# Kernel tuning notes

Measured on AMD Instinct MI355X. Metric: run time of the kernel, lower is better.

Reference implementation:

```python
import jax, jax.numpy as jnp
import numpy as np

VOCAB, EMB, HID, OUT = 1000, 256, 512, 1
NUM_IN, NUM_OUT = 7, 4
B, S = 64, 512
D = EMB + NUM_OUT  # conv input dim = 260


def setup_inputs() -> dict:
    key = jax.random.key(0)
    ks = jax.random.split(key, 8)
    ev = jax.random.randint(ks[0], (B, S, 1), 0, VOCAB).astype(jnp.float32)
    num = jax.random.normal(ks[1], (B, S, NUM_IN), jnp.float32)
    X = jnp.concatenate([ev, num], axis=-1)  # [B,S,8]; col 0 = event ids
    def w(k, shape, fan_in):
        return jax.random.normal(k, shape, jnp.float32) / np.sqrt(fan_in).astype(np.float32)
    return {
        "X": X,
        "emb": w(ks[2], (VOCAB, EMB), EMB),
        "Wn": w(ks[3], (NUM_IN, NUM_OUT), NUM_IN), "bn": jnp.zeros((NUM_OUT,), jnp.float32),
        "Wf": w(ks[4], (D, 3 * HID), D), "bf": jnp.zeros((3 * HID,), jnp.float32),
        "Wb": w(ks[5], (D, 3 * HID), D), "bb": jnp.zeros((3 * HID,), jnp.float32),
        "Wo": w(ks[6], (2 * HID, OUT), 2 * HID), "bo": jnp.zeros((OUT,), jnp.float32),
    }


def _fo_pool(Z, F):
    # Z, F: [S, B, H]. Linear recurrence h_t = F_t * h_{t-1} + (1 - F_t) * Z_t.
    def step(h, zf):
        z, f = zf
        h = f * h + (1.0 - f) * z
        return h, h
    h0 = jnp.zeros(Z.shape[1:], Z.dtype)
    _, hs = jax.lax.scan(step, h0, (Z, F))
    return hs  # [S, B, H]


def _forward(X, emb, Wn, bn, Wf, bf, Wb, bb, Wo, bo):
    ev = jax.lax.stop_gradient(X[:, :, 0]).astype(jnp.int32)  # event-type ids
    num = X[:, :, 1:]
    e = emb[ev]                          # [B,S,EMB]
    n = num @ Wn + bn                    # [B,S,NUM_OUT]
    c = jnp.concatenate([e, n], axis=-1)  # [B,S,D]

    def gates(W, b):
        g = jnp.einsum('bsd,dk->sbk', c, W) + b  # kernel-1 conv == GEMM; [S,B,3H]
        Z, F = g[..., :HID], g[..., HID:2 * HID]  # O gate is computed but unused upstream
        return jnp.tanh(Z), jax.nn.sigmoid(F)

    Zf, Ff = gates(Wf, bf)
    Zb, Fb = gates(Wb, bb)
    hf = _fo_pool(Zf, Ff)                       # forward direction
    hb = _fo_pool(Zb[::-1], Fb[::-1])[::-1]     # backward: scan reversed, re-reverse
    # torch takes h_combined[-1]: last forward state, first backward-scan state
    final = jnp.concatenate([hf[-1], hb[-1]], axis=-1)  # [B, 2H]
    return final @ Wo + bo  # dropout p=0 is identity


def reference(X, emb, Wn, bn, Wf, bf, Wb, bb, Wo, bo):
    return _forward(X, emb, Wn, bn, Wf, bf, Wb, bb, Wo, bo)
```

## Files before the change

### kernel.cpp

```cpp
#include <hip/hip_runtime.h>
#include <stdint.h>

#define B_ 64
#define S_ 512
#define EMB_ 256
#define NIN_ 7
#define NOUT_ 4
#define HID_ 512
#define VOCAB_ 1000
#define VP_ 1024
#define NG_ 2048

typedef __bf16 bf16x8 __attribute__((ext_vector_type(8)));
typedef float floatx4 __attribute__((ext_vector_type(4)));
typedef unsigned short u16x8 __attribute__((ext_vector_type(8)));

__device__ __forceinline__ unsigned short f2bf(float f) {
    unsigned u = __float_as_uint(f);
    u += 0x7FFFu + ((u >> 16) & 1u);
    return (unsigned short)(u >> 16);
}
__device__ __forceinline__ float bf2f(unsigned short h) {
    return __uint_as_float(((unsigned)h) << 16);
}
__device__ __forceinline__ float rcp_(float x) { return __builtin_amdgcn_rcpf(x); }
__device__ __forceinline__ float exp2_(float x) {
    float r; asm("v_exp_f32 %0, %1" : "=v"(r) : "v"(x)); return r;
}
#define L2E_ 1.4426950408889634f
__device__ __forceinline__ float sigmoidf_(float x) {
    return rcp_(1.0f + exp2_(x * (-L2E_)));
}
__device__ __forceinline__ float tanhf_(float x) {
    float ax = fabsf(x);
    float e = exp2_(ax * (-2.0f * L2E_));
    float t = (1.0f - e) * rcp_(1.0f + e);
    return copysignf(t, x);
}


__global__ __launch_bounds__(256) void prep(
    const float* __restrict__ emb, const float* __restrict__ bn,
    const float* __restrict__ Wf, const float* __restrict__ bfv,
    const float* __restrict__ Wb, const float* __restrict__ bb,
    unsigned short* __restrict__ Aemb, unsigned short* __restrict__ WT,
    float* __restrict__ W4, float* __restrict__ bvec) {
    int bid = blockIdx.x;
    int tid = threadIdx.x;

    if (bid < 64) {
        int g = bid;
#pragma unroll
        for (int half = 0; half < 2; ++half) {
            int t = tid + 256 * half;
            int r15 = t & 15;
            int kchunk = (t >> 4) & 3;
            int kt = t >> 6;
            int row = g * 16 + r15;
            int k0 = kt * 32 + kchunk * 8;
            unsigned short p[8];
            if (row < VOCAB_) {
                float4 a = *(const float4*)(emb + (size_t)row * EMB_ + k0);
                float4 b = *(const float4*)(emb + (size_t)row * EMB_ + k0 + 4);
                p[0]=f2bf(a.x); p[1]=f2bf(a.y); p[2]=f2bf(a.z); p[3]=f2bf(a.w);
                p[4]=f2bf(b.x); p[5]=f2bf(b.y); p[6]=f2bf(b.z); p[7]=f2bf(b.w);
            } else {
#pragma unroll
                for (int q = 0; q < 8; ++q) p[q] = 0;
            }
            size_t chunk = ((size_t)(g >> 3) * 8 + kt) * 8 + (g & 7);
            *(u16x8*)(Aemb + chunk * 512 + (16 * kchunk + r15) * 8) =
                *(const u16x8*)p;
        }
    } else if (bid < 192) {
        __shared__ float raw[32][132];
        int job = bid - 64;
        int idx = job >> 3;
        int kt  = job & 7;
        int p = idx >> 3;
        int gq = idx & 7;
        const float* W = p ? Wb : Wf;
        int j0 = gq * 64;
        int r = tid >> 3;
        int i = tid & 7;
        int k0 = kt * 32;

        const float* src = W + (size_t)(k0 + r) * 1536;
        float4 a0 = *(const float4*)(src + j0 + i * 8);
        float4 a1 = *(const float4*)(src + j0 + i * 8 + 4);
        float4 b0 = *(const float4*)(src + 512 + j0 + i * 8);
        float4 b1 = *(const float4*)(src + 512 + j0 + i * 8 + 4);
        *(float4*)&raw[r][i * 8]          = a0;
        *(float4*)&raw[r][i * 8 + 4]      = a1;
        *(float4*)&raw[r][64 + i * 8]     = b0;
        *(float4*)&raw[r][64 + i * 8 + 4] = b1;
        __syncthreads();
#pragma unroll
        for (int h = 0; h < 2; ++h) {
            int e = tid + 256 * h;
            int gl = e >> 6;
            int rest = e & 63;
            int kchunk = rest >> 4;
            int v15 = rest & 15;
            int joff = gl * 8 + (v15 >> 1);
            int cl = joff + 64 * (v15 & 1);
            unsigned short pk[8];
#pragma unroll
            for (int q = 0; q < 8; ++q) pk[q] = f2bf(raw[kchunk * 8 + q][cl]);
            int g = p * 64 + gq * 8 + gl;
            size_t chunk = ((size_t)(g >> 3) * 8 + kt) * 8 + (g & 7);
            *(u16x8*)(WT + chunk * 512 + (16 * kchunk + v15) * 8) =
                *(const u16x8*)pk;
        }
    } else {
        int v = (bid - 192) * 256 + tid;
        int part = v >> 10;
        int m = v & 1023;
        int j = m >> 1;
        int c = (m & 1) ? (512 + j) : j;
        const float* W = part ? Wb : Wf;
        float bv = part ? bb[c] : bfv[c];
#pragma unroll
        for (int q = 0; q < NOUT_; ++q) {
            float w = W[(size_t)(256 + q) * 1536 + c];
            W4[(size_t)q * NG_ + v] = w;
            bv = fmaf(bn[q], w, bv);
        }
        bvec[v] = bv;
    }
}

__global__ __launch_bounds__(256) void gemmG(
    const unsigned short* __restrict__ Aemb, const unsigned short* __restrict__ WT,
    const float* __restrict__ bvec, unsigned short* __restrict__ G) {
    int bid = blockIdx.x;
    int mtile = bid & 7;
    int ntile = bid >> 3;
    int r0 = mtile * 128;
    int n0 = ntile * 128;
    int tid = threadIdx.x;
    int lane = tid & 63, wave = tid >> 6;
    int wm = wave & 1, wn = wave >> 1;
    int rl = lane & 15;

    const unsigned short* pa = Aemb + ((size_t)mtile * 64 + 4 * wm) * 512 + lane * 8;
    const unsigned short* pb = WT + ((size_t)ntile * 64 + 4 * wn) * 512 + lane * 8;

    floatx4 acc[4][4];
#pragma unroll
    for (int mi = 0; mi < 4; ++mi)
#pragma unroll
        for (int ni = 0; ni < 4; ++ni) acc[mi][ni] = (floatx4){0.f, 0.f, 0.f, 0.f};

    bf16x8 afc[4], bfc[4], afn[4], bfn[4];
#pragma unroll
    for (int mi = 0; mi < 4; ++mi) afc[mi] = *(const bf16x8*)(pa + mi * 512);
#pragma unroll
    for (int ni = 0; ni < 4; ++ni) bfc[ni] = *(const bf16x8*)(pb + ni * 512);

#pragma unroll
    for (int kt = 0; kt < 8; ++kt) {
        if (kt < 7) {
#pragma unroll
            for (int mi = 0; mi < 4; ++mi)
                afn[mi] = *(const bf16x8*)(pa + (size_t)(kt + 1) * 4096 + mi * 512);
#pragma unroll
            for (int ni = 0; ni < 4; ++ni)
                bfn[ni] = *(const bf16x8*)(pb + (size_t)(kt + 1) * 4096 + ni * 512);
        }
#pragma unroll
        for (int mi = 0; mi < 4; ++mi)
#pragma unroll
            for (int ni = 0; ni < 4; ++ni)
                acc[mi][ni] = __builtin_amdgcn_mfma_f32_16x16x32_bf16(afc[mi], bfc[ni], acc[mi][ni], 0, 0, 0);
        if (kt < 7) {
#pragma unroll
            for (int mi = 0; mi < 4; ++mi) afc[mi] = afn[mi];
#pragma unroll
            for (int ni = 0; ni < 4; ++ni) bfc[ni] = bfn[ni];
        }
    }

#pragma unroll
    for (int ni = 0; ni < 4; ++ni) {
        int n = n0 + 64 * wn + 16 * ni + rl;
        float bv = bvec[n];
#pragma unroll
        for (int mi = 0; mi < 4; ++mi) {
            int rb = r0 + 64 * wm + 16 * mi + (lane >> 4) * 4;
#pragma unroll
            for (int v = 0; v < 4; ++v)
                G[(size_t)(rb + v) * NG_ + n] = f2bf(acc[mi][ni][v] + bv);
        }
    }
}

__global__ __launch_bounds__(512) void scan(
    const float* __restrict__ X, const unsigned short* __restrict__ G,
    const float* __restrict__ W4, const float* __restrict__ Wn,
    float* __restrict__ PQ) {
    __shared__ float LX[512];
    __shared__ float LN[64][4];
    __shared__ int   LO[64];
    int bid = blockIdx.x;
    int b = bid >> 3, chunk = bid & 7;
    int s0 = chunk * 64;
    int j = threadIdx.x;

    LX[j] = X[((size_t)b * S_ + s0 + (j >> 3)) * 8 + (j & 7)];
    __syncthreads();

    if (j < 64) LO[j] = (int)LX[j * 8] * (NG_ * 2);
    if (j < 256) {
        int t = j >> 2, q = j & 3;
        float s = 0.f;
#pragma unroll
        for (int i = 0; i < NIN_; ++i) s = fmaf(LX[t * 8 + 1 + i], Wn[i * NOUT_ + q], s);
        LN[t][q] = s;
    }

    float2 w4p[NOUT_];
#pragma unroll
    for (int q = 0; q < NOUT_; ++q)
        w4p[q] = *(const float2*)(W4 + (size_t)q * NG_ + 2 * j);
    __syncthreads();

    const char* Gb = (const char*)G + 4 * j;
    unsigned gp[8];
#pragma unroll
    for (int r = 0; r < 8; ++r)
        gp[r] = *(const unsigned*)(Gb + LO[r]);

    float P = 1.f, Q = 0.f;
#pragma unroll 8
    for (int s = 0; s < 64; ++s) {
        unsigned gpc = gp[s & 7];
        if (s < 56)
            gp[s & 7] = *(const unsigned*)(Gb + LO[s + 8]);
        float gz = bf2f((unsigned short)(gpc & 0xffffu));
        float gf = bf2f((unsigned short)(gpc >> 16));
        float4 n4 = *(const float4*)(&LN[s][0]);
        gz = fmaf(n4.x, w4p[0].x, gz);
        gz = fmaf(n4.y, w4p[1].x, gz);
        gz = fmaf(n4.z, w4p[2].x, gz);
        gz = fmaf(n4.w, w4p[3].x, gz);
        gf = fmaf(n4.x, w4p[0].y, gf);
        gf = fmaf(n4.y, w4p[1].y, gf);
        gf = fmaf(n4.z, w4p[2].y, gf);
        gf = fmaf(n4.w, w4p[3].y, gf);
        float z = tanhf_(gz);
        float f = sigmoidf_(gf);
        Q = fmaf(f, Q - z, z);
        P *= f;
    }
    ((float2*)PQ)[(size_t)bid * 512 + j] = make_float2(P, Q);
}

__global__ __launch_bounds__(512) void final_out(
    const float* __restrict__ X, const unsigned short* __restrict__ G,
    const float* __restrict__ W4, const float* __restrict__ Wn,
    const float* __restrict__ Wo, const float* __restrict__ bo,
    const float* __restrict__ PQ, float* __restrict__ out) {
    int b = blockIdx.x;
    int j = threadIdx.x;

    float h = 0.f;
#pragma unroll
    for (int c = 0; c < 8; ++c) {
        float2 pq = ((const float2*)PQ)[((size_t)b * 8 + c) * 512 + j];
        h = fmaf(pq.x, h, pq.y);
    }

    const float* xr = X + ((size_t)b * S_ + (S_ - 1)) * 8;
    int ev = (int)xr[0];
    float n4[NOUT_];
#pragma unroll
    for (int q = 0; q < NOUT_; ++q) {
        float s = 0.f;
#pragma unroll
        for (int i = 0; i < NIN_; ++i) s = fmaf(xr[1 + i], Wn[i * NOUT_ + q], s);
        n4[q] = s;
    }
    unsigned gpc = *(const unsigned*)(G + (size_t)ev * NG_ + 1024 + 2 * j);
    float gz = bf2f((unsigned short)(gpc & 0xffffu));
    float gf = bf2f((unsigned short)(gpc >> 16));
#pragma unroll
    for (int q = 0; q < NOUT_; ++q) {
        float2 w = *(const float2*)(W4 + (size_t)q * NG_ + 1024 + 2 * j);
        gz = fmaf(n4[q], w.x, gz);
        gf = fmaf(n4[q], w.y, gf);
    }
    float hb = (1.f - sigmoidf_(gf)) * tanhf_(gz);

    float partial = fmaf(h, Wo[j], hb * Wo[512 + j]);
#pragma unroll
    for (int off = 32; off > 0; off >>= 1)
        partial += __shfl_down(partial, off);
    __shared__ float red[8];
    if ((j & 63) == 0) red[j >> 6] = partial;
    __syncthreads();
    if (j == 0) {
        float s = bo[0];
#pragma unroll
        for (int w = 0; w < 8; ++w) s += red[w];
        out[b] = s;
    }
}

extern "C" void kernel_launch(void* const* d_in, const int* in_sizes, int n_in,
                              void* d_out, int out_size, void* d_ws, size_t ws_size,
                              hipStream_t stream) {
    const float* X   = (const float*)d_in[0];
    const float* emb = (const float*)d_in[1];
    const float* Wn  = (const float*)d_in[2];
    const float* bn  = (const float*)d_in[3];
    const float* Wf  = (const float*)d_in[4];
    const float* bfv = (const float*)d_in[5];
    const float* Wb  = (const float*)d_in[6];
    const float* bb  = (const float*)d_in[7];
    const float* Wo  = (const float*)d_in[8];
    const float* bo  = (const float*)d_in[9];
    float* out = (float*)d_out;

    size_t off_A  = 0;
    size_t off_WT = off_A  + (size_t)VP_ * EMB_ * 2;
    size_t off_G  = off_WT + (size_t)NG_ * EMB_ * 2;
    size_t off_W4 = off_G  + (size_t)VP_ * NG_ * 2;
    size_t off_bv = off_W4 + (size_t)NOUT_ * NG_ * 4;
    size_t off_PQ = off_bv + (size_t)NG_ * 4;
    size_t need   = off_PQ + (size_t)B_ * 8 * 512 * 2 * sizeof(float);
    if (ws_size < need) return;

    unsigned short* Aemb = (unsigned short*)((char*)d_ws + off_A);
    unsigned short* WT   = (unsigned short*)((char*)d_ws + off_WT);
    unsigned short* G    = (unsigned short*)((char*)d_ws + off_G);
    float*          W4   = (float*)((char*)d_ws + off_W4);
    float*          bvec = (float*)((char*)d_ws + off_bv);
    float*          PQ   = (float*)((char*)d_ws + off_PQ);

    prep<<<200, 256, 0, stream>>>(emb, bn, Wf, bfv, Wb, bb, Aemb, WT, W4, bvec);
    gemmG<<<128, 256, 0, stream>>>(Aemb, WT, bvec, G);
    scan<<<512, 512, 0, stream>>>(X, G, W4, Wn, PQ);
    final_out<<<64, 512, 0, stream>>>(X, G, W4, Wn, Wo, bo, PQ, out);
}
```

Baseline: 110.9 us.

## Compute backward gates only for final tokens and fuse final reduction into scan

```diff
diff --git a/kernel.cpp b/kernel.cpp
--- a/kernel.cpp
+++ b/kernel.cpp
@@ -14,6 +14,7 @@
 typedef __bf16 bf16x8 __attribute__((ext_vector_type(8)));
 typedef float floatx4 __attribute__((ext_vector_type(4)));
 typedef unsigned short u16x8 __attribute__((ext_vector_type(8)));
+typedef unsigned long long ull;
 
 __device__ __forceinline__ unsigned short f2bf(float f) {
     unsigned u = __float_as_uint(f);
@@ -44,7 +45,8 @@
     const float* __restrict__ Wf, const float* __restrict__ bfv,
     const float* __restrict__ Wb, const float* __restrict__ bb,
     unsigned short* __restrict__ Aemb, unsigned short* __restrict__ WT,
-    float* __restrict__ W4, float* __restrict__ bvec) {
+    float* __restrict__ W4, float* __restrict__ bvec,
+    unsigned* __restrict__ bcnt) {
     int bid = blockIdx.x;
     int tid = threadIdx.x;
 
@@ -127,81 +129,142 @@
             bv = fmaf(bn[q], w, bv);
         }
         bvec[v] = bv;
+        if (bid == 192 && tid < 64) bcnt[tid] = 0;
     }
 }
 
 __global__ __launch_bounds__(256) void gemmG(
+    const float* __restrict__ X,
     const unsigned short* __restrict__ Aemb, const unsigned short* __restrict__ WT,
-    const float* __restrict__ bvec, unsigned short* __restrict__ G) {
+    const float* __restrict__ bvec,
+    unsigned short* __restrict__ G1, unsigned short* __restrict__ Gb) {
     int bid = blockIdx.x;
-    int mtile = bid & 7;
-    int ntile = bid >> 3;
-    int r0 = mtile * 128;
-    int n0 = ntile * 128;
     int tid = threadIdx.x;
     int lane = tid & 63, wave = tid >> 6;
-    int wm = wave & 1, wn = wave >> 1;
     int rl = lane & 15;
 
-    const unsigned short* pa = Aemb + ((size_t)mtile * 64 + 4 * wm) * 512 + lane * 8;
-    const unsigned short* pb = WT + ((size_t)ntile * 64 + 4 * wn) * 512 + lane * 8;
-
-    floatx4 acc[4][4];
-#pragma unroll
-    for (int mi = 0; mi < 4; ++mi)
-#pragma unroll
-        for (int ni = 0; ni < 4; ++ni) acc[mi][ni] = (floatx4){0.f, 0.f, 0.f, 0.f};
-
-    bf16x8 afc[4], bfc[4], afn[4], bfn[4];
-#pragma unroll
-    for (int mi = 0; mi < 4; ++mi) afc[mi] = *(const bf16x8*)(pa + mi * 512);
-#pragma unroll
-    for (int ni = 0; ni < 4; ++ni) bfc[ni] = *(const bf16x8*)(pb + ni * 512);
-
-#pragma unroll
-    for (int kt = 0; kt < 8; ++kt) {
-        if (kt < 7) {
+    if (bid < 64) {
+        int mtile = bid & 7;
+        int ntile = bid >> 3;
+        int r0 = mtile * 128;
+        int n0 = ntile * 128;
+        int wm = wave & 1, wn = wave >> 1;
+
+        const unsigned short* pa = Aemb + ((size_t)mtile * 64 + 4 * wm) * 512 + lane * 8;
+        const unsigned short* pb = WT + ((size_t)ntile * 64 + 4 * wn) * 512 + lane * 8;
+
+        floatx4 acc[4][4];
+#pragma unroll
+        for (int mi = 0; mi < 4; ++mi)
+#pragma unroll
+            for (int ni = 0; ni < 4; ++ni) acc[mi][ni] = (floatx4){0.f, 0.f, 0.f, 0.f};
+
+        bf16x8 afc[4], bfc[4], afn[4], bfn[4];
+#pragma unroll
+        for (int mi = 0; mi < 4; ++mi) afc[mi] = *(const bf16x8*)(pa + mi * 512);
+#pragma unroll
+        for (int ni = 0; ni < 4; ++ni) bfc[ni] = *(const bf16x8*)(pb + ni * 512);
+
+#pragma unroll
+        for (int kt = 0; kt < 8; ++kt) {
+            if (kt < 7) {
+#pragma unroll
+                for (int mi = 0; mi < 4; ++mi)
+                    afn[mi] = *(const bf16x8*)(pa + (size_t)(kt + 1) * 4096 + mi * 512);
+#pragma unroll
+                for (int ni = 0; ni < 4; ++ni)
+                    bfn[ni] = *(const bf16x8*)(pb + (size_t)(kt + 1) * 4096 + ni * 512);
+            }
 #pragma unroll
             for (int mi = 0; mi < 4; ++mi)
-                afn[mi] = *(const bf16x8*)(pa + (size_t)(kt + 1) * 4096 + mi * 512);
-#pragma unroll
-            for (int ni = 0; ni < 4; ++ni)
-                bfn[ni] = *(const bf16x8*)(pb + (size_t)(kt + 1) * 4096 + ni * 512);
-        }
+#pragma unroll
+                for (int ni = 0; ni < 4; ++ni)
+                    acc[mi][ni] = __builtin_amdgcn_mfma_f32_16x16x32_bf16(afc[mi], bfc[ni], acc[mi][ni], 0, 0, 0);
+            if (kt < 7) {
+#pragma unroll
+                for (int mi = 0; mi < 4; ++mi) afc[mi] = afn[mi];
+#pragma unroll
+                for (int ni = 0; ni < 4; ++ni) bfc[ni] = bfn[ni];
+            }
+        }
+
+#pragma unroll
+        for (int ni = 0; ni < 4; ++ni) {
+            int n = n0 + 64 * wn + 16 * ni + rl;
+            float bv = bvec[n];
+#pragma unroll
+            for (int mi = 0; mi < 4; ++mi) {
+                int rb = r0 + 64 * wm + 16 * mi + (lane >> 4) * 4;
+#pragma unroll
+                for (int v = 0; v < 4; ++v)
+                    G1[(size_t)(rb + v) * 1024 + n] = f2bf(acc[mi][ni][v] + bv);
+            }
+        }
+    } else {
+        __shared__ int evs[64];
+        int ntile = bid - 64;
+        int n0 = ntile * 128;
+        if (tid < 64)
+            evs[tid] = (int)X[((size_t)tid * S_ + (S_ - 1)) * 8];
+        __syncthreads();
+
+        int cbase[4];
+#pragma unroll
+        for (int mi = 0; mi < 4; ++mi) {
+            int R = evs[16 * mi + rl];
+            int g = R >> 4;
+            cbase[mi] = (g >> 3) * 32768 + (g & 7) * 512 + (lane >> 4) * 128 + (R & 15) * 8;
+        }
+        const unsigned short* pb = WT + ((size_t)(8 + ntile) * 64 + 2 * wave) * 512 + lane * 8;
+
+        floatx4 acc[4][2];
 #pragma unroll
         for (int mi = 0; mi < 4; ++mi)
 #pragma unroll
-            for (int ni = 0; ni < 4; ++ni)
-                acc[mi][ni] = __builtin_amdgcn_mfma_f32_16x16x32_bf16(afc[mi], bfc[ni], acc[mi][ni], 0, 0, 0);
-        if (kt < 7) {
-#pragma unroll
-            for (int mi = 0; mi < 4; ++mi) afc[mi] = afn[mi];
-#pragma unroll
-            for (int ni = 0; ni < 4; ++ni) bfc[ni] = bfn[ni];
-        }
-    }
-
-#pragma unroll
-    for (int ni = 0; ni < 4; ++ni) {
-        int n = n0 + 64 * wn + 16 * ni + rl;
-        float bv = bvec[n];
-#pragma unroll
-        for (int mi = 0; mi < 4; ++mi) {
-            int rb = r0 + 64 * wm + 16 * mi + (lane >> 4) * 4;
-#pragma unroll
-            for (int v = 0; v < 4; ++v)
-                G[(size_t)(rb + v) * NG_ + n] = f2bf(acc[mi][ni][v] + bv);
-        }
-    }
-}
-
-__global__ __launch_bounds__(512) void scan(
-    const float* __restrict__ X, const unsigned short* __restrict__ G,
-    const float* __restrict__ W4, const float* __restrict__ Wn,
-    float* __restrict__ PQ) {
+            for (int ni = 0; ni < 2; ++ni) acc[mi][ni] = (floatx4){0.f, 0.f, 0.f, 0.f};
+
+#pragma unroll
+        for (int kt = 0; kt < 8; ++kt) {
+            bf16x8 afc[4], bfc[2];
+#pragma unroll
+            for (int mi = 0; mi < 4; ++mi)
+                afc[mi] = *(const bf16x8*)(Aemb + (size_t)cbase[mi] + (size_t)kt * 4096);
+#pragma unroll
+            for (int ni = 0; ni < 2; ++ni)
+                bfc[ni] = *(const bf16x8*)(pb + (size_t)kt * 4096 + ni * 512);
+#pragma unroll
+            for (int mi = 0; mi < 4; ++mi)
+#pragma unroll
+                for (int ni = 0; ni < 2; ++ni)
+                    acc[mi][ni] = __builtin_amdgcn_mfma_f32_16x16x32_bf16(afc[mi], bfc[ni], acc[mi][ni], 0, 0, 0);
+        }
+
+#pragma unroll
+        for (int ni = 0; ni < 2; ++ni) {
+            int n = n0 + 32 * wave + 16 * ni + rl;
+            float bv = bvec[1024 + n];
+#pragma unroll
+            for (int mi = 0; mi < 4; ++mi) {
+                int rb = 16 * mi + (lane >> 4) * 4;
+#pragma unroll
+                for (int v = 0; v < 4; ++v)
+                    Gb[(size_t)(rb + v) * 1024 + n] = f2bf(acc[mi][ni][v] + bv);
+            }
+        }
+    }
+}
+
+__global__ __launch_bounds__(512) void scanF(
+    const float* __restrict__ X, const unsigned short* __restrict__ G1,
+    const unsigned short* __restrict__ Gb, const float* __restrict__ W4,
+    const float* __restrict__ Wn, const float* __restrict__ Wo,
+    const float* __restrict__ bo, float* __restrict__ PQ,
+    unsigned* __restrict__ bcnt, float* __restrict__ out) {
     __shared__ float LX[512];
     __shared__ float LN[64][4];
     __shared__ int   LO[64];
+    __shared__ unsigned lastf;
+    __shared__ float red[8];
     int bid = blockIdx.x;
     int b = bid >> 3, chunk = bid & 7;
     int s0 = chunk * 64;
@@ -210,7 +273,7 @@
     LX[j] = X[((size_t)b * S_ + s0 + (j >> 3)) * 8 + (j & 7)];
     __syncthreads();
 
-    if (j < 64) LO[j] = (int)LX[j * 8] * (NG_ * 2);
+    if (j < 64) LO[j] = (int)LX[j * 8] * 2048;
     if (j < 256) {
         int t = j >> 2, q = j & 3;
         float s = 0.f;
@@ -225,18 +288,18 @@
         w4p[q] = *(const float2*)(W4 + (size_t)q * NG_ + 2 * j);
     __syncthreads();
 
-    const char* Gb = (const char*)G + 4 * j;
+    const char* Gbase = (const char*)G1 + 4 * j;
     unsigned gp[8];
 #pragma unroll
     for (int r = 0; r < 8; ++r)
-        gp[r] = *(const unsigned*)(Gb + LO[r]);
+        gp[r] = *(const unsigned*)(Gbase + LO[r]);
 
     float P = 1.f, Q = 0.f;
 #pragma unroll 8
     for (int s = 0; s < 64; ++s) {
         unsigned gpc = gp[s & 7];
         if (s < 56)
-            gp[s & 7] = *(const unsigned*)(Gb + LO[s + 8]);
+            gp[s & 7] = *(const unsigned*)(Gbase + LO[s + 8]);
         float gz = bf2f((unsigned short)(gpc & 0xffffu));
         float gf = bf2f((unsigned short)(gpc >> 16));
         float4 n4 = *(const float4*)(&LN[s][0]);
@@ -253,57 +316,63 @@
         Q = fmaf(f, Q - z, z);
         P *= f;
     }
-    ((float2*)PQ)[(size_t)bid * 512 + j] = make_float2(P, Q);
-}
-
-__global__ __launch_bounds__(512) void final_out(
-    const float* __restrict__ X, const unsigned short* __restrict__ G,
-    const float* __restrict__ W4, const float* __restrict__ Wn,
-    const float* __restrict__ Wo, const float* __restrict__ bo,
-    const float* __restrict__ PQ, float* __restrict__ out) {
-    int b = blockIdx.x;
-    int j = threadIdx.x;
-
-    float h = 0.f;
-#pragma unroll
-    for (int c = 0; c < 8; ++c) {
-        float2 pq = ((const float2*)PQ)[((size_t)b * 8 + c) * 512 + j];
-        h = fmaf(pq.x, h, pq.y);
-    }
-
-    const float* xr = X + ((size_t)b * S_ + (S_ - 1)) * 8;
-    int ev = (int)xr[0];
-    float n4[NOUT_];
-#pragma unroll
-    for (int q = 0; q < NOUT_; ++q) {
-        float s = 0.f;
-#pragma unroll
-        for (int i = 0; i < NIN_; ++i) s = fmaf(xr[1 + i], Wn[i * NOUT_ + q], s);
-        n4[q] = s;
-    }
-    unsigned gpc = *(const unsigned*)(G + (size_t)ev * NG_ + 1024 + 2 * j);
-    float gz = bf2f((unsigned short)(gpc & 0xffffu));
-    float gf = bf2f((unsigned short)(gpc >> 16));
-#pragma unroll
-    for (int q = 0; q < NOUT_; ++q) {
-        float2 w = *(const float2*)(W4 + (size_t)q * NG_ + 1024 + 2 * j);
-        gz = fmaf(n4[q], w.x, gz);
-        gf = fmaf(n4[q], w.y, gf);
-    }
-    float hb = (1.f - sigmoidf_(gf)) * tanhf_(gz);
-
-    float partial = fmaf(h, Wo[j], hb * Wo[512 + j]);
-#pragma unroll
-    for (int off = 32; off > 0; off >>= 1)
-        partial += __shfl_down(partial, off);
-    __shared__ float red[8];
-    if ((j & 63) == 0) red[j >> 6] = partial;
+    {
+        union { float2 f; ull q; } pv;
+        pv.f = make_float2(P, Q);
+        __hip_atomic_store((ull*)PQ + (size_t)bid * 512 + j, pv.q,
+                           __ATOMIC_RELAXED, __HIP_MEMORY_SCOPE_AGENT);
+    }
+
     __syncthreads();
     if (j == 0) {
-        float s = bo[0];
-#pragma unroll
-        for (int w = 0; w < 8; ++w) s += red[w];
-        out[b] = s;
+        unsigned old = __hip_atomic_fetch_add(bcnt + b, 1u, __ATOMIC_RELAXED,
+                                              __HIP_MEMORY_SCOPE_AGENT);
+        lastf = (old == 7u);
+    }
+    __syncthreads();
+
+    if (lastf) {
+        float h = 0.f;
+#pragma unroll
+        for (int c = 0; c < 8; ++c) {
+            union { float2 f; ull q; } pv;
+            pv.q = __hip_atomic_load((const ull*)PQ + ((size_t)b * 8 + c) * 512 + j,
+                                     __ATOMIC_RELAXED, __HIP_MEMORY_SCOPE_AGENT);
+            h = fmaf(pv.f.x, h, pv.f.y);
+        }
+
+        const float* xr = X + ((size_t)b * S_ + (S_ - 1)) * 8;
+        float n4[NOUT_];
+#pragma unroll
+        for (int q = 0; q < NOUT_; ++q) {
+            float s = 0.f;
+#pragma unroll
+            for (int i = 0; i < NIN_; ++i) s = fmaf(xr[1 + i], Wn[i * NOUT_ + q], s);
+            n4[q] = s;
+        }
+        unsigned gpc = *(const unsigned*)(Gb + (size_t)b * 1024 + 2 * j);
+        float gz = bf2f((unsigned short)(gpc & 0xffffu));
+        float gf = bf2f((unsigned short)(gpc >> 16));
+#pragma unroll
+        for (int q = 0; q < NOUT_; ++q) {
+            float2 w = *(const float2*)(W4 + (size_t)q * NG_ + 1024 + 2 * j);
+            gz = fmaf(n4[q], w.x, gz);
+            gf = fmaf(n4[q], w.y, gf);
+        }
+        float hb = (1.f - sigmoidf_(gf)) * tanhf_(gz);
+
+        float partial = fmaf(h, Wo[j], hb * Wo[512 + j]);
+#pragma unroll
+        for (int off = 32; off > 0; off >>= 1)
+            partial += __shfl_down(partial, off);
+        if ((j & 63) == 0) red[j >> 6] = partial;
+        __syncthreads();
+        if (j == 0) {
+            float s = bo[0];
+#pragma unroll
+            for (int w = 0; w < 8; ++w) s += red[w];
+            out[b] = s;
+        }
     }
 }
 
@@ -324,22 +393,25 @@
 
     size_t off_A  = 0;
     size_t off_WT = off_A  + (size_t)VP_ * EMB_ * 2;
-    size_t off_G  = off_WT + (size_t)NG_ * EMB_ * 2;
-    size_t off_W4 = off_G  + (size_t)VP_ * NG_ * 2;
+    size_t off_G1 = off_WT + (size_t)NG_ * EMB_ * 2;
+    size_t off_Gb = off_G1 + (size_t)VP_ * 1024 * 2;
+    size_t off_W4 = off_Gb + (size_t)B_ * 1024 * 2;
     size_t off_bv = off_W4 + (size_t)NOUT_ * NG_ * 4;
     size_t off_PQ = off_bv + (size_t)NG_ * 4;
-    size_t need   = off_PQ + (size_t)B_ * 8 * 512 * 2 * sizeof(float);
+    size_t off_bc = off_PQ + (size_t)B_ * 8 * 512 * 2 * sizeof(float);
+    size_t need   = off_bc + 64 * sizeof(unsigned);
     if (ws_size < need) return;
 
     unsigned short* Aemb = (unsigned short*)((char*)d_ws + off_A);
     unsigned short* WT   = (unsigned short*)((char*)d_ws + off_WT);
-    unsigned short* G    = (unsigned short*)((char*)d_ws + off_G);
+    unsigned short* G1   = (unsigned short*)((char*)d_ws + off_G1);
+    unsigned short* Gb   = (unsigned short*)((char*)d_ws + off_Gb);
     float*          W4   = (float*)((char*)d_ws + off_W4);
     float*          bvec = (float*)((char*)d_ws + off_bv);
     float*          PQ   = (float*)((char*)d_ws + off_PQ);
-
-    prep<<<200, 256, 0, stream>>>(emb, bn, Wf, bfv, Wb, bb, Aemb, WT, W4, bvec);
-    gemmG<<<128, 256, 0, stream>>>(Aemb, WT, bvec, G);
-    scan<<<512, 512, 0, stream>>>(X, G, W4, Wn, PQ);
-    final_out<<<64, 512, 0, stream>>>(X, G, W4, Wn, Wo, bo, PQ, out);
-}
+    unsigned*       bcnt = (unsigned*)((char*)d_ws + off_bc);
+
+    prep<<<200, 256, 0, stream>>>(emb, bn, Wf, bfv, Wb, bb, Aemb, WT, W4, bvec, bcnt);
+    gemmG<<<72, 256, 0, stream>>>(X, Aemb, WT, bvec, G1, Gb);
+    scanF<<<512, 512, 0, stream>>>(X, G1, Gb, W4, Wn, Wo, bo, PQ, bcnt, out);
+}
```

New measurement: 110.7 us. No clear change (-0.2%).
